# Kernel optimization log

Hardware: AMD Instinct MI355X
Metric: run time of the kernel (lower is better)

Reference implementation:

```python
import jax, jax.numpy as jnp
import numpy as np
from jax import lax


def setup_inputs() -> dict:
    key = jax.random.key(0)
    k1, k2 = jax.random.split(key)
    B, H, T, F, R = 8, 16, 4096, 64, 65
    a = jax.random.normal(k1, (B, H, T, R), dtype=jnp.float32)
    v = jax.random.normal(k2, (B, H, T, F), dtype=jnp.float32)
    return {"a": a, "v": v}


def _unfold_matmul(a, v):
    # out[b,h,t,f] = sum_r a[b,h,t,r] * v[b,h, t + r - R//2, f]  (zero-padded in time)
    B, H, T, F = v.shape
    R = a.shape[-1]
    pad = R // 2
    vp = jnp.pad(v, ((0, 0), (0, 0), (pad, pad), (0, 0)))  # (B,H,T+R-1,F)

    def body(acc, r):
        vs = lax.dynamic_slice_in_dim(vp, r, T, axis=2)      # shifted values (B,H,T,F)
        ar = lax.dynamic_slice_in_dim(a, r, 1, axis=3)       # (B,H,T,1)
        return acc + ar * vs, None

    out, _ = lax.scan(body, jnp.zeros_like(v), jnp.arange(R))
    return out


def reference(a, v):
    return _unfold_matmul(a, v)
```

## Files before the change

### kernel.cpp

```cpp
#include <hip/hip_runtime.h>


#define TT 4096
#define RRR 65
#define FF 64
#define TILE 64
#define SA_S 100
#define SV_S 132
#define NTPB 8

typedef short bf16x8 __attribute__((ext_vector_type(8)));
typedef float f32x16 __attribute__((ext_vector_type(16)));

__device__ __forceinline__ unsigned short f2bf(float x) {
    unsigned int u = __float_as_uint(x);
    u += 0x7fff + ((u >> 16) & 1);
    return (unsigned short)(u >> 16);
}
__device__ __forceinline__ unsigned pk2(float lo, float hi) {
    return (unsigned)f2bf(lo) | ((unsigned)f2bf(hi) << 16);
}

__global__ __launch_bounds__(256, 4)
void unfold_mfma(const float* __restrict__ a, const float* __restrict__ v,
                 float* __restrict__ out) {
    __shared__ __align__(16) unsigned short sa[TILE * SA_S];
    __shared__ __align__(16) unsigned short sv[FF * SV_S];

    const int tid = threadIdx.x;
    const int f   = tid & 63;
    const int wv  = tid >> 6;

    const int bh = blockIdx.x >> 3;
    const float* vsl = v + (size_t)bh * TT * FF;
    const size_t obase = (size_t)bh * TT * FF;

    {
        uint4 z = make_uint4(0, 0, 0, 0);
        uint4* sp = (uint4*)sa;
        #pragma unroll
        for (int it = 0; it < 4; ++it) {
            int lin = tid + it * 256;
            if (lin < (TILE * SA_S) / 8) sp[lin] = z;
        }
    }

    float4 aq[4];
    float  ae[2];
    float  vv[8][4];

    int t0 = ((blockIdx.x & 7) * NTPB) << 6;
    const float* arow = a + ((size_t)bh * TT + t0) * RRR;

#define ISSUE_LOADS() do {                                                     \
    _Pragma("unroll")                                                          \
    for (int it = 0; it < 4; ++it) {                                           \
        int lin = tid + it * 256;                                              \
        if (lin < TILE * 15) {                                                 \
            int R = lin / 15, j = lin - R * 15;                                \
            int r0 = (4 - (R & 3)) & 3;                                        \
            aq[it] = *(const float4*)(arow + (size_t)R * RRR + r0 + 4 * j);    \
        }                                                                      \
    }                                                                          \
    _Pragma("unroll")                                                          \
    for (int it = 0; it < 2; ++it) {                                           \
        int lin = tid + it * 256;                                              \
        if (lin < TILE * 5) {                                                  \
            int R = lin / 5, e = lin - R * 5;                                  \
            int r0 = (4 - (R & 3)) & 3;                                        \
            int r = (e < r0) ? e : 60 + e;                                     \
            ae[it] = arow[(size_t)R * RRR + r];                                \
        }                                                                      \
    }                                                                          \
    {                                                                          \
        const int gb = t0 - 32 + 32 * wv;                                      \
        if (t0 >= 32 && t0 + 96 <= TT) {                                       \
            _Pragma("unroll")                                                  \
            for (int it = 0; it < 8; ++it)                                     \
                _Pragma("unroll")                                              \
                for (int j = 0; j < 4; ++j)                                    \
                    vv[it][j] = vsl[(size_t)(gb + 4 * it + j) * FF + f];       \
        } else {                                                               \
            _Pragma("unroll")                                                  \
            for (int it = 0; it < 8; ++it)                                     \
                _Pragma("unroll")                                              \
                for (int j = 0; j < 4; ++j) {                                  \
                    int g = gb + 4 * it + j;                                   \
                    vv[it][j] = (g >= 0 && g < TT)                             \
                                ? vsl[(size_t)g * FF + f] : 0.f;               \
                }                                                              \
        }                                                                      \
    }                                                                          \
} while (0)

#define SCATTER() do {                                                         \
    _Pragma("unroll")                                                          \
    for (int it = 0; it < 4; ++it) {                                           \
        int lin = tid + it * 256;                                              \
        if (lin < TILE * 15) {                                                 \
            int R = lin / 15, j = lin - R * 15;                                \
            int r0 = (4 - (R & 3)) & 3;                                        \
            int rq = r0 + 4 * j;                                               \
            float4 q = aq[it];                                                 \
            uint2 pw; pw.x = pk2(q.x, q.y); pw.y = pk2(q.z, q.w);              \
            *(uint2*)&sa[R * SA_S + (R & 31) + rq] = pw;                       \
        }                                                                      \
    }                                                                          \
    _Pragma("unroll")                                                          \
    for (int it = 0; it < 2; ++it) {                                           \
        int lin = tid + it * 256;                                              \
        if (lin < TILE * 5) {                                                  \
            int R = lin / 5, e = lin - R * 5;                                  \
            int r0 = (4 - (R & 3)) & 3;                                        \
            int r = (e < r0) ? e : 60 + e;                                     \
            sa[R * SA_S + (R & 31) + r] = f2bf(ae[it]);                        \
        }                                                                      \
    }                                                                          \
    _Pragma("unroll")                                                          \
    for (int it = 0; it < 8; ++it) {                                           \
        uint2 pw; pw.x = pk2(vv[it][0], vv[it][1]);                            \
        pw.y = pk2(vv[it][2], vv[it][3]);                                      \
        *(uint2*)&sv[f * SV_S + 32 * wv + 4 * it] = pw;                        \
    }                                                                          \
} while (0)

    ISSUE_LOADS();
    __syncthreads();

    const int n  = f & 31;
    const int hi = f >> 5;
    const int wr = wv >> 1;
    const int wc = wv & 1;
    const int Rw = 32 * wr + n;

    #pragma unroll 1
    for (int i = 0; i < NTPB; ++i) {
        SCATTER();
        const int cur_t0 = t0;
        __syncthreads();

        if (i + 1 < NTPB) {
            t0 += TILE;
            arow = a + ((size_t)bh * TT + t0) * RRR;
            ISSUE_LOADS();
        }

        f32x16 acc = {};
        #pragma unroll
        for (int kb = 0; kb < 6; ++kb) {
            const int cp = kb * 16 + hi * 8;
            bf16x8 af = *(const bf16x8*)&sa[Rw * SA_S + cp];
            bf16x8 bv = *(const bf16x8*)&sv[(32 * wc + n) * SV_S + (32 * wr + cp)];
            acc = __builtin_amdgcn_mfma_f32_32x32x16_bf16(af, bv, acc, 0, 0, 0);
        }

        float* op = out + obase + (size_t)(cur_t0 + 32 * wr) * FF + 32 * wc;
        #pragma unroll
        for (int reg = 0; reg < 16; ++reg) {
            int row = (reg & 3) + 8 * (reg >> 2) + 4 * hi;
            __builtin_nontemporal_store(acc[reg], &op[row * FF + n]);
        }
        __syncthreads();
    }
}

extern "C" void kernel_launch(void* const* d_in, const int* in_sizes, int n_in,
                              void* d_out, int out_size, void* d_ws, size_t ws_size,
                              hipStream_t stream) {
    const float* a = (const float*)d_in[0];
    const float* v = (const float*)d_in[1];
    float* out = (float*)d_out;

    const int BH = in_sizes[1] / (TT * FF);
    const int grid = BH * (TT / TILE) / NTPB;

    unfold_mfma<<<grid, 256, 0, stream>>>(a, v, out);
}
```

Before: 75.46 us.

## Use ring buffer for V halo across tiles and halve tiles per block

The V shared buffer becomes a 128-column ring indexed modulo RM, so each tile loads only its 64 new time rows instead of reloading the full 128-row halo window. This removes the redundant V global loads that came from the overlapping halo. Tiles per block drop from 8 to 4, which doubles the grid, and the occupancy hint rises to 5 blocks. In exchange there is extra index masking, and each block now pays its halo prologue once over only 4 tiles.

```diff
diff --git a/kernel.cpp b/kernel.cpp
--- a/kernel.cpp
+++ b/kernel.cpp
@@ -7,7 +7,8 @@
 #define TILE 64
 #define SA_S 100
 #define SV_S 132
-#define NTPB 8
+#define NTPB 4
+#define RM 127
 
 typedef short bf16x8 __attribute__((ext_vector_type(8)));
 typedef float f32x16 __attribute__((ext_vector_type(16)));
@@ -21,7 +22,7 @@
     return (unsigned)f2bf(lo) | ((unsigned)f2bf(hi) << 16);
 }
 
-__global__ __launch_bounds__(256, 4)
+__global__ __launch_bounds__(256, 5)
 void unfold_mfma(const float* __restrict__ a, const float* __restrict__ v,
                  float* __restrict__ out) {
     __shared__ __align__(16) unsigned short sa[TILE * SA_S];
@@ -31,7 +32,9 @@
     const int f   = tid & 63;
     const int wv  = tid >> 6;
 
-    const int bh = blockIdx.x >> 3;
+    const int bh = blockIdx.x >> 4;
+    const int T0 = (blockIdx.x & 15) << 8;
+
     const float* vsl = v + (size_t)bh * TT * FF;
     const size_t obase = (size_t)bh * TT * FF;
 
@@ -47,12 +50,12 @@
 
     float4 aq[4];
     float  ae[2];
-    float  vv[8][4];
-
-    int t0 = ((blockIdx.x & 7) * NTPB) << 6;
+    float  vv[4][4];
+
+    int t0 = T0;
     const float* arow = a + ((size_t)bh * TT + t0) * RRR;
 
-#define ISSUE_LOADS() do {                                                     \
+#define ISSUE_A() do {                                                         \
     _Pragma("unroll")                                                          \
     for (int it = 0; it < 4; ++it) {                                           \
         int lin = tid + it * 256;                                              \
@@ -72,28 +75,28 @@
             ae[it] = arow[(size_t)R * RRR + r];                                \
         }                                                                      \
     }                                                                          \
-    {                                                                          \
-        const int gb = t0 - 32 + 32 * wv;                                      \
-        if (t0 >= 32 && t0 + 96 <= TT) {                                       \
+} while (0)
+
+#define ISSUE_V(s0) do {                                                       \
+    const int gb = (s0) + 16 * wv;                                             \
+    if ((s0) + 64 <= TT) {                                                     \
+        _Pragma("unroll")                                                      \
+        for (int it = 0; it < 4; ++it)                                         \
             _Pragma("unroll")                                                  \
-            for (int it = 0; it < 8; ++it)                                     \
-                _Pragma("unroll")                                              \
-                for (int j = 0; j < 4; ++j)                                    \
-                    vv[it][j] = vsl[(size_t)(gb + 4 * it + j) * FF + f];       \
-        } else {                                                               \
+            for (int j = 0; j < 4; ++j)                                        \
+                vv[it][j] = vsl[(size_t)(gb + 4 * it + j) * FF + f];           \
+    } else {                                                                   \
+        _Pragma("unroll")                                                      \
+        for (int it = 0; it < 4; ++it)                                         \
             _Pragma("unroll")                                                  \
-            for (int it = 0; it < 8; ++it)                                     \
-                _Pragma("unroll")                                              \
-                for (int j = 0; j < 4; ++j) {                                  \
-                    int g = gb + 4 * it + j;                                   \
-                    vv[it][j] = (g >= 0 && g < TT)                             \
-                                ? vsl[(size_t)g * FF + f] : 0.f;               \
-                }                                                              \
-        }                                                                      \
-    }                                                                          \
-} while (0)
-
-#define SCATTER() do {                                                         \
+            for (int j = 0; j < 4; ++j) {                                      \
+                int g = gb + 4 * it + j;                                       \
+                vv[it][j] = (g < TT) ? vsl[(size_t)g * FF + f] : 0.f;          \
+            }                                                                  \
+    }                                                                          \
+} while (0)
+
+#define SCAT_A() do {                                                          \
     _Pragma("unroll")                                                          \
     for (int it = 0; it < 4; ++it) {                                           \
         int lin = tid + it * 256;                                              \
@@ -116,15 +119,44 @@
             sa[R * SA_S + (R & 31) + r] = f2bf(ae[it]);                        \
         }                                                                      \
     }                                                                          \
-    _Pragma("unroll")                                                          \
-    for (int it = 0; it < 8; ++it) {                                           \
+} while (0)
+
+#define SCAT_V(s0) do {                                                        \
+    const int cb = (s0) + 16 * wv;                                             \
+    _Pragma("unroll")                                                          \
+    for (int it = 0; it < 4; ++it) {                                           \
         uint2 pw; pw.x = pk2(vv[it][0], vv[it][1]);                            \
         pw.y = pk2(vv[it][2], vv[it][3]);                                      \
-        *(uint2*)&sv[f * SV_S + 32 * wv + 4 * it] = pw;                        \
-    }                                                                          \
-} while (0)
-
-    ISSUE_LOADS();
+        *(uint2*)&sv[f * SV_S + ((cb + 4 * it) & RM)] = pw;                    \
+    }                                                                          \
+} while (0)
+
+    ISSUE_A();
+    {
+        float pv[8][4];
+        const int gb = T0 - 32 + 32 * wv;
+        if (T0 >= 32) {
+            #pragma unroll
+            for (int it = 0; it < 8; ++it)
+                #pragma unroll
+                for (int j = 0; j < 4; ++j)
+                    pv[it][j] = vsl[(size_t)(gb + 4 * it + j) * FF + f];
+        } else {
+            #pragma unroll
+            for (int it = 0; it < 8; ++it)
+                #pragma unroll
+                for (int j = 0; j < 4; ++j) {
+                    int g = gb + 4 * it + j;
+                    pv[it][j] = (g >= 0) ? vsl[(size_t)g * FF + f] : 0.f;
+                }
+        }
+        #pragma unroll
+        for (int it = 0; it < 8; ++it) {
+            uint2 pw; pw.x = pk2(pv[it][0], pv[it][1]);
+            pw.y = pk2(pv[it][2], pv[it][3]);
+            *(uint2*)&sv[f * SV_S + ((gb + 4 * it) & RM)] = pw;
+        }
+    }
     __syncthreads();
 
     const int n  = f & 31;
@@ -135,22 +167,26 @@
 
     #pragma unroll 1
     for (int i = 0; i < NTPB; ++i) {
-        SCATTER();
+        SCAT_A();
+        if (i > 0) SCAT_V(t0 + 32);
         const int cur_t0 = t0;
         __syncthreads();
 
         if (i + 1 < NTPB) {
             t0 += TILE;
             arow = a + ((size_t)bh * TT + t0) * RRR;
-            ISSUE_LOADS();
-        }
-
+            ISSUE_A();
+            ISSUE_V(cur_t0 + 96);
+        }
+
+        const int cbase = (cur_t0 - 32) & RM;
         f32x16 acc = {};
         #pragma unroll
         for (int kb = 0; kb < 6; ++kb) {
             const int cp = kb * 16 + hi * 8;
             bf16x8 af = *(const bf16x8*)&sa[Rw * SA_S + cp];
-            bf16x8 bv = *(const bf16x8*)&sv[(32 * wc + n) * SV_S + (32 * wr + cp)];
+            bf16x8 bv = *(const bf16x8*)&sv[(32 * wc + n) * SV_S
+                                            + ((cbase + 32 * wr + cp) & RM)];
             acc = __builtin_amdgcn_mfma_f32_32x32x16_bf16(af, bv, acc, 0, 0, 0);
         }
 
```

New measurement: 78.68 us. 1.04x slower.
